# Kernel optimization log

Hardware: AMD Instinct MI355X
Metric: run time of the kernel (lower is better)

The kernel has to match this reference:

```python
import jax, jax.numpy as jnp
import numpy as np

B, T, H = 512, 32, 300


def setup_inputs() -> dict:
    key = jax.random.key(0)
    ks = jax.random.split(key, 24)
    u = lambda k, shape: jax.random.uniform(k, shape, jnp.float32, -0.1, 0.1)
    return {
        'local_inputs': jax.random.normal(ks[0], (B, T, 28, 10), jnp.float32),
        'labels': jax.random.normal(ks[1], (B, T, 1, 1), jnp.float32),
        'extras': jax.random.normal(ks[2], (B, T, 4, 1), jnp.float32),
        'DisM': jax.random.normal(ks[3], (10,), jnp.float32),
        'AngleM': jax.random.uniform(ks[4], (10,), jnp.float32, 0.0, 360.0),
        'Wih': u(ks[5], (10, 4 * H, 11)),
        'b_ih': u(ks[6], (10, 4 * H)),
        'b_hh': u(ks[7], (10, 4 * H)),
        'Wt': u(ks[8], (4 * H, 4)),
        'bt_ih': u(ks[9], (4 * H,)),
        'bt_hh': u(ks[10], (4 * H,)),
        'wp': u(ks[11], (H, 2 * H)),
        'bp': u(ks[12], (H, 1)),
        'F1': u(ks[13], (2 * H, 200)),
        'b1': u(ks[14], (200,)),
        'F2': u(ks[15], (202, 1)),
        'b2': u(ks[16], (1,)),
        'ff': u(ks[17], (100, 17)),
        'bff': u(ks[18], (100, 1)),
        'fuse1': u(ks[19], (H, 100)),
        'biasf': u(ks[20], (100,)),
        'Wout': u(ks[21], (100, 1)),
        'biasout': u(ks[22], (1,)),
        'a': u(ks[23], (1,)),
    }


def reference(local_inputs, labels, extras, DisM, AngleM,
              Wih, b_ih, b_hh, Wt, bt_ih, bt_hh,
              wp, bp, F1, b1, F2, b2, ff, bff,
              fuse1, biasf, Wout, biasout, a):
    x = jnp.transpose(local_inputs, (1, 0, 2, 3))   # [T,B,28,10]
    exs = jnp.transpose(extras, (1, 0, 2, 3))       # [T,B,4,1]
    labels_r = jnp.transpose(labels, (1, 0, 2, 3)).reshape(T, B, 1)
    b_cells = b_ih + b_hh                            # weight_hh * 0 vanishes; biases remain
    bt = bt_ih + bt_hh
    wA = jax.nn.softmax(DisM)                        # [10] static distance weights
    aa = a[0]

    def cells(s):  # s: [B,11,10] -> con [B,H,10]; zero-state LSTMCell per neighbor
        g = jnp.einsum('kgi,bik->bkg', Wih, s) + b_cells  # [B,10,4H]
        i, f, gg, o = jnp.split(g, 4, axis=-1)
        h = jax.nn.sigmoid(o) * jnp.tanh(jax.nn.sigmoid(i) * jnp.tanh(gg))
        return jnp.transpose(h, (0, 2, 1))

    def target_cell(t):  # [B,4] -> [B,H]
        g = t @ Wt.T + bt
        i, f, gg, o = jnp.split(g, 4, axis=-1)
        return jax.nn.sigmoid(o) * jnp.tanh(jax.nn.sigmoid(i) * jnp.tanh(gg))

    def attend_predict(fl, con1, htarget):
        # fl: [B,28,10], con1: [B,H,10]
        hcat = jnp.concatenate([jnp.transpose(con1, (0, 2, 1)),
                                jnp.broadcast_to(htarget[:, None, :], (B, 10, H))], axis=2)  # [B,10,2H]
        fc1 = jax.nn.relu(jnp.einsum('bkh,ho->bko', hcat, F1) + b1)          # [B,10,200]
        ang = jnp.abs(fl[:, 10, :] - AngleM[None, :]) / 360.0                # [B,10]
        fc2 = jnp.concatenate([fc1, fl[:, 8, :, None], ang[..., None]], axis=2)  # [B,10,202]
        wdyn = jax.nn.relu(jnp.einsum('bko,od->bkd', fc2, F2)[..., 0] + b2[0])   # [B,10]
        # faithful to the original: softmax over neighbors of [10,B], then FLAT reshape to [B,1,10]
        wa3 = jax.nn.softmax(wdyn.T, axis=0).reshape(B, 1, 10)
        cat = jnp.sum(con1 * wa3, axis=2)                                    # [B,H]
        flin2 = jnp.einsum('of,bfk->bok', ff, fl[:, 11:, :]) + bff           # [B,100,10]
        fusiondis = jnp.sum(flin2 * wA[None, None, :], axis=2)               # [B,100]
        fuse = cat @ fuse1 + biasf                                           # [B,100]
        return (aa * fuse + (1.0 - aa) * fusiondis) @ Wout + biasout         # [B,1]

    # t = 0: con1 = con (no lastcon yet)
    con0 = cells(x[0, :, :11, :])
    p0 = attend_predict(x[0], con0, target_cell(exs[0, :, :4, 0]))

    def step(lastcon, inp):
        fl, e = inp
        con = cells(fl[:, :11, :])
        ht = target_cell(e[:, :4, 0])
        con1 = jax.nn.relu(jnp.einsum('oh,bhk->bok', wp,
                                      jnp.concatenate([con, lastcon], axis=1)) + bp)  # [B,H,10]
        return con, attend_predict(fl, con1, ht)

    _, preds = jax.lax.scan(step, con0, (x[1:], exs[1:]))
    preds = jnp.concatenate([p0[None], preds], axis=0)  # [T,B,1]
    return preds, labels_r
```

## Files before the change

kernel.cpp:

```cpp
#include <hip/hip_runtime.h>
#include <hip/hip_bf16.h>


#define TB 3
#define NBT 171
#define NR 32
#define NTHR 512
#define NW 8
#define KP 616
#define TBF 16

#define OFF_SM    0
#define OFF_WBF2  163840
#define OFF_F1S   256256
#define OFF_WCELL 319488
#define OFF_BTP   392448
#define OFF_WTP   393348
#define OFF_F1F   396948
#define OFF_WA    414868
#define OFF_SWA   414878
#define BASE_U32  414880
#define CON1_BYTE ((size_t)BASE_U32 * 4)
#define CONG_BYTE (CON1_BYTE + (size_t)98304000)
#define WS_NEED_BYTES (CONG_BYTE + (size_t)98304000)

typedef __attribute__((ext_vector_type(8))) short s16x8;
typedef __attribute__((ext_vector_type(4))) float f32x4;
typedef unsigned short u16;

__device__ __forceinline__ float rcpf(float x){ return __builtin_amdgcn_rcpf(x); }
__device__ __forceinline__ float sigf(float x){ return rcpf(1.0f+__expf(-x)); }
__device__ __forceinline__ float tanhf_(float x){ return 1.0f - 2.0f*rcpf(__expf(2.0f*x)+1.0f); }
__device__ __forceinline__ float bfu(u16 u){ return __uint_as_float(((unsigned)u)<<16); }
__device__ __forceinline__ u16 f2us(float f){ return (u16)(__float_as_uint(f)>>16); }
__device__ __forceinline__ u16 f2usr(float f){
  __hip_bfloat16 h = __float2bfloat16(f);
  return *(u16*)&h;
}

__global__ __launch_bounds__(256,4) void kern_cells(
    const float* __restrict__ li, const float* wsf, u16* __restrict__ cong)
{
  __shared__ __align__(16) float xs[64][12];
  const int tid=threadIdx.x, k=blockIdx.x;
  const int tbase = blockIdx.y*64;
  const int t = tbase>>9, bg0 = tbase&511;
  for (int p=tid; p<64*11; p+=256){
    int r=p/11, i=p%11;
    xs[r][i] = li[(((size_t)(bg0+r)*32+t)*28+i)*10+k];
  }
  if (tid<64) xs[tid][11] = 1.0f;
  __syncthreads();
  const int w = tid>>6, lane = tid&63, lo=lane&15, qd=lane>>4;
  short av[8];
  #pragma unroll
  for (int j=0;j<8;j++){
    int kk = qd*8+j;
    float v = (kk<12)? xs[w*16+lo][kk] : 0.f;
    av[j] = (short)f2usr(v);
  }
  s16x8 Ax = (s16x8){av[0],av[1],av[2],av[3],av[4],av[5],av[6],av[7]};
  const unsigned* wc = (const unsigned*)wsf + OFF_WCELL;
  const s16x8 Z = (s16x8){0,0,0,0,0,0,0,0};
  for (int ht=0; ht<19; ht++){
    s16x8 Bi=Z, Bg=Z, Bo=Z;
    if (qd<2){
      const unsigned* bb = wc + (((k*19+ht)*3)*32 + qd*16+lo)*4;
      Bi = *(const s16x8*)(bb);
      Bg = *(const s16x8*)(bb + 32*4);
      Bo = *(const s16x8*)(bb + 64*4);
    }
    f32x4 gi={0.f,0.f,0.f,0.f}, gg={0.f,0.f,0.f,0.f}, go={0.f,0.f,0.f,0.f};
    gi = __builtin_amdgcn_mfma_f32_16x16x32_bf16(Ax, Bi, gi, 0,0,0);
    gg = __builtin_amdgcn_mfma_f32_16x16x32_bf16(Ax, Bg, gg, 0,0,0);
    go = __builtin_amdgcn_mfma_f32_16x16x32_bf16(Ax, Bo, go, 0,0,0);
    int h = ht*16+lo;
    if (h<300){
      #pragma unroll
      for (int r=0;r<4;r++){
        float hv = sigf(go[r]) * tanhf_( sigf(gi[r]) * tanhf_(gg[r]) );
        int tb = tbase + w*16 + qd*4 + r;
        cong[((size_t)tb*10+k)*300 + h] = f2usr(hv);
      }
    }
  }
}

__global__ __launch_bounds__(NTHR,8) void kern_main_split(
    const float* __restrict__ li, const float* __restrict__ exs,
    const float* __restrict__ AngleM, const float* __restrict__ bp,
    const float* __restrict__ F2, const float* __restrict__ b2,
    const float* wsf, unsigned* __restrict__ con1u, float* smg,
    const u16* __restrict__ cong)
{
  __shared__ __align__(16) u16 cct[NR][KP];
  __shared__ float xse[TB][2][10];
  __shared__ float exss[TB][4];
  __shared__ float wdP[NW][NR];
  __shared__ float wdL[NR];
  const int tid = threadIdx.x;
  const int t = blockIdx.y, bt = blockIdx.x, b0 = bt*TB;
  const int w = tid>>6, lane = tid&63, lo = lane&15, qd = lane>>4;

  for (int p=tid;p<TB*20;p+=NTHR){
    int b=p/20, r=p%20, rr=r/10, k=r%10;
    int bg = b0+b; if (bg>511) bg=511;
    xse[b][rr][k] = li[((bg*32+t)*28 + (rr?10:8))*10 + k];
  }
  for (int p=tid;p<TB*4;p+=NTHR){
    int b=p/4, e=p%4;
    int bg = b0+b; if (bg>511) bg=511;
    exss[b][e] = exs[(bg*32+t)*4+e];
  }
  for (int p=tid; p<30*4; p+=NTHR){
    int n=p/4, c=p%4;
    ((unsigned*)&cct[n][600])[c] = 0u;
  }
  __syncthreads();

  const int nh = (t==0)?1:2;
  for (int p=tid; p<nh*TB*750; p+=NTHR){
    int half=p/(TB*750), r=p%(TB*750), n=r/75, op=r%75;
    int tp = half? t-1 : t;
    int bg = b0 + n/10; if (bg>511) bg=511;
    uint2 v = *(const uint2*)((const unsigned*)cong +
                ((size_t)(tp*512+bg)*10 + n%10)*150 + 2*op);
    *(uint2*)((unsigned*)&cct[n][300*half] + 2*op) = v;
  }
  __syncthreads();

  f32x4 acc[3][2];
  #pragma unroll
  for (int i=0;i<3;i++)
    #pragma unroll
    for (int nt=0;nt<2;nt++) acc[i][nt] = (f32x4){0.f,0.f,0.f,0.f};
  if (t>0){
    const u16* wbfA = (const u16*)((const unsigned*)wsf + OFF_WBF2);
    for (int ks=0; ks<19; ks++){
      const int kb = ks*32 + qd*8;
      s16x8 Bv[2];
      #pragma unroll
      for (int nt=0;nt<2;nt++)
        Bv[nt] = *(const s16x8*)&cct[nt*16+lo][kb];
      #pragma unroll
      for (int i=0;i<3;i++){
        int mt = i*8+w;
        if (mt<19){
          s16x8 Av = *(const s16x8*)(wbfA + ((size_t)(mt*19+ks)*64 + lane)*8);
          #pragma unroll
          for (int nt=0;nt<2;nt++)
            acc[i][nt] = __builtin_amdgcn_mfma_f32_16x16x32_bf16(Av, Bv[nt], acc[i][nt], 0,0,0);
        }
      }
    }
  }
  __syncthreads();

  if (t>0){
    #pragma unroll
    for (int i=0;i<3;i++){
      int mt = i*8+w;
      if (mt<19 && (mt<18 || qd<3)){
        int ob = mt*16 + qd*4;
        float p0=bp[ob], p1=bp[ob+1], p2=bp[ob+2], p3=bp[ob+3];
        #pragma unroll
        for (int nt=0;nt<2;nt++){
          int n = nt*16+lo;
          float v0=acc[i][nt][0]+p0, v1=acc[i][nt][1]+p1,
                v2=acc[i][nt][2]+p2, v3=acc[i][nt][3]+p3;
          unsigned w0 = ((unsigned)f2us(v1>0.f?v1:0.f)<<16) | f2us(v0>0.f?v0:0.f);
          unsigned w1 = ((unsigned)f2us(v3>0.f?v3:0.f)<<16) | f2us(v2>0.f?v2:0.f);
          *(unsigned*)&cct[n][ob]   = w0;
          *(unsigned*)&cct[n][ob+2] = w1;
        }
      }
    }
  }
  for (int p=tid; p<TB*75; p+=NTHR){
    int b=p/75, q=p%75, o=4*q;
    f32x4 ai={0.f,0.f,0.f,0.f}, ag={0.f,0.f,0.f,0.f}, ao={0.f,0.f,0.f,0.f};
    #pragma unroll
    for (int e=0;e<4;e++){
      float xv = exss[b][e];
      f32x4 wi = *(const f32x4*)&wsf[OFF_WTP+(e*3+0)*300+o];
      f32x4 wg = *(const f32x4*)&wsf[OFF_WTP+(e*3+1)*300+o];
      f32x4 wo = *(const f32x4*)&wsf[OFF_WTP+(e*3+2)*300+o];
      #pragma unroll
      for (int c=0;c<4;c++){
        ai[c] += wi[c]*xv; ag[c] += wg[c]*xv; ao[c] += wo[c]*xv;
      }
    }
    f32x4 bi = *(const f32x4*)&wsf[OFF_BTP+o];
    f32x4 bg = *(const f32x4*)&wsf[OFF_BTP+300+o];
    f32x4 bo = *(const f32x4*)&wsf[OFF_BTP+600+o];
    u16 u[4];
    #pragma unroll
    for (int c=0;c<4;c++){
      float vi = ai[c]+bi[c], vg = ag[c]+bg[c], vo = ao[c]+bo[c];
      u[c] = f2usr( sigf(vo)*tanhf_(sigf(vi)*tanhf_(vg)) );
    }
    uint2 pk;
    pk.x = ((unsigned)u[1]<<16) | u[0];
    pk.y = ((unsigned)u[3]<<16) | u[2];
    #pragma unroll
    for (int k=0;k<10;k++)
      *(uint2*)&cct[b*10+k][300+o] = pk;
  }
  for (int p=tid; p<30*4; p+=NTHR){
    int n=p/4, c=p%4;
    ((unsigned*)&cct[n][600])[c] = (c==0)? 0x00003f80u : 0u;
  }
  __syncthreads();

  for (int p=tid; p<TB*750; p+=NTHR){
    int n=p/75, op=p%75;
    int bg = b0 + n/10;
    if (bg < 512){
      uint2 v = *(const uint2*)((unsigned*)&cct[n][0] + 2*op);
      *(uint2*)(con1u + ((size_t)(t*512+bg)*10 + n%10)*150 + 2*op) = v;
    }
  }

  f32x4 acc2[2][2];
  #pragma unroll
  for (int mt=0;mt<2;mt++)
    #pragma unroll
    for (int j=0;j<2;j++) acc2[mt][j] = (f32x4){0.f,0.f,0.f,0.f};
  {
    const u16* f1s = (const u16*)((const unsigned*)wsf + OFF_F1S);
    for (int ks=0; ks<19; ks++){
      const int kb = ks*32 + qd*8;
      s16x8 Am[2];
      #pragma unroll
      for (int mt=0;mt<2;mt++)
        Am[mt] = *(const s16x8*)&cct[mt*16+lo][kb];
      #pragma unroll
      for (int j=0;j<2;j++){
        int nt = w + j*8;
        if (nt<13){
          s16x8 Bf = *(const s16x8*)(f1s + ((size_t)(nt*19+ks)*64 + lane)*8);
          #pragma unroll
          for (int mt=0;mt<2;mt++)
            acc2[mt][j] = __builtin_amdgcn_mfma_f32_16x16x32_bf16(Am[mt], Bf, acc2[mt][j], 0,0,0);
        }
      }
    }
  }
  {
    float f2c[2];
    #pragma unroll
    for (int j=0;j<2;j++){
      int nt = w + j*8;
      int jj = nt*16+lo;
      f2c[j] = (nt<13 && jj<200)? F2[jj] : 0.f;
    }
    #pragma unroll
    for (int mt=0;mt<2;mt++)
      #pragma unroll
      for (int r=0;r<4;r++){
        float s = 0.f;
        #pragma unroll
        for (int j=0;j<2;j++){
          float v = acc2[mt][j][r];
          s += (v>0.f? v:0.f) * f2c[j];
        }
        s += __shfl_xor(s,1,64); s += __shfl_xor(s,2,64);
        s += __shfl_xor(s,4,64); s += __shfl_xor(s,8,64);
        if (lo==0) wdP[w][mt*16+qd*4+r] = s;
      }
  }
  __syncthreads();
  if (tid<TB*10){
    int n=tid, b=n/10, k=n%10;
    float v = 0.f;
    #pragma unroll
    for (int ww=0;ww<NW;ww++) v += wdP[ww][n];
    float ang = fabsf(xse[b][1][k]-AngleM[k]) * (1.0f/360.0f);
    v += xse[b][0][k]*F2[200] + ang*F2[201] + b2[0];
    wdL[n] = v>0.f? v : 0.f;
  }
  __syncthreads();
  if (tid<TB && b0+tid < 512){
    int b=tid;
    float m = wdL[b*10];
    #pragma unroll
    for (int k=1;k<10;k++) m = fmaxf(m, wdL[b*10+k]);
    float e[10]; float s=0.f;
    #pragma unroll
    for (int k=0;k<10;k++){ e[k]=__expf(wdL[b*10+k]-m); s+=e[k]; }
    float inv = rcpf(s);
    #pragma unroll
    for (int k=0;k<10;k++) smg[t*5120 + k*512 + b0+b] = e[k]*inv;
  }
}

__global__ __launch_bounds__(NTHR,8) void kern_final(
    const float* __restrict__ li, const float* __restrict__ labels,
    const float* __restrict__ ff, const float* __restrict__ bff,
    const float* __restrict__ biasf, const float* __restrict__ Wout,
    const float* __restrict__ biasout, const float* __restrict__ a,
    const float* wsf, const unsigned* __restrict__ con1u,
    float* __restrict__ outp)
{
  __shared__ __align__(16) float cats[TBF][324];
  __shared__ __align__(16) float xs17[TBF][17][10];
  __shared__ float wa3s[TBF][10];
  __shared__ float dss[TBF][17];
  __shared__ float wAs[10];
  __shared__ float part[7][TBF];
  const int tid=threadIdx.x, t=blockIdx.y, bt=blockIdx.x, b0=bt*TBF;
  const int w = tid>>6, lane = tid&63, lo = lane&15, qd = lane>>4;
  if (tid>=NTHR-TBF){
    int b = tid-(NTHR-TBF);
    outp[16384 + t*512 + b0+b] = labels[(b0+b)*32+t];
  }
  for (int p=tid;p<TBF*85;p+=NTHR){
    int b=p/85, r=p%85, f=r/5, pr=r%5;
    *(float2*)&xs17[b][f][2*pr] =
        *(const float2*)&li[(((b0+b)*32+t)*28 + 11+f)*10 + 2*pr];
  }
  if (tid<10) wAs[tid] = wsf[OFF_WA+tid];
  for (int p=tid;p<TBF*10;p+=NTHR){
    int b=p/10, k=p%10;
    int g = (b0+b)*10+k;
    wa3s[b][k] = wsf[OFF_SM + t*5120 + (g>>9)*512 + (g&511)];
  }
  __syncthreads();
  for (int p=tid;p<TBF*17;p+=NTHR){
    int b=p/17, f=p%17; float s=0.f;
    #pragma unroll
    for (int k=0;k<10;k++) s += xs17[b][f][k]*wAs[k];
    dss[b][f]=s;
  }
  for (int p=tid;p<TBF*75;p+=NTHR){
    int b=p/75, q=p%75, o=4*q;
    const unsigned* base = con1u + ((size_t)(t*512 + b0+b)*10)*150 + 2*q;
    f32x4 s = {0.f,0.f,0.f,0.f};
    #pragma unroll
    for (int k=0;k<10;k++){
      uint2 cv = *(const uint2*)(base + (size_t)k*150);
      float wk = wa3s[b][k];
      s[0] += bfu((u16)(cv.x & 0xffffu))*wk;
      s[1] += bfu((u16)(cv.x >> 16))*wk;
      s[2] += bfu((u16)(cv.y & 0xffffu))*wk;
      s[3] += bfu((u16)(cv.y >> 16))*wk;
    }
    *(f32x4*)&cats[b][o] = s;
  }
  for (int p=tid;p<TBF*6;p+=NTHR){
    int b=p/6, c=p%6;
    *(f32x4*)&cats[b][300+4*c] = (f32x4){0.f,0.f,0.f,0.f};
  }
  __syncthreads();
  if (w < 7){
    f32x4 D = (f32x4){0.f,0.f,0.f,0.f};
    const u16* f1f = (const u16*)((const unsigned*)wsf + OFF_F1F);
    for (int ks=0; ks<10; ks++){
      const int kb = ks*32 + qd*8;
      f32x4 c0 = *(const f32x4*)&cats[lo][kb];
      f32x4 c1 = *(const f32x4*)&cats[lo][kb+4];
      short av[8];
      #pragma unroll
      for (int j=0;j<4;j++){
        av[j]   = (short)f2usr(c0[j]);
        av[4+j] = (short)f2usr(c1[j]);
      }
      s16x8 Ax = (s16x8){av[0],av[1],av[2],av[3],av[4],av[5],av[6],av[7]};
      s16x8 Bf = *(const s16x8*)(f1f + ((size_t)(w*10+ks)*64 + lane)*8);
      D = __builtin_amdgcn_mfma_f32_16x16x32_bf16(Ax, Bf, D, 0,0,0);
    }
    {
      int o = w*16+lo;
      bool ov = o<100;
      float aa = a[0], swa = wsf[OFF_SWA];
      float bfo = ov? biasf[o] : 0.f;
      float bffo = ov? bff[o]*swa : 0.f;
      float wo = ov? Wout[o] : 0.f;
      #pragma unroll
      for (int r=0;r<4;r++){
        int b = qd*4+r;
        float fu = D[r] + bfo;
        float fd = bffo;
        if (ov){
          #pragma unroll
          for (int f=0;f<17;f++) fd += ff[o*17+f]*dss[b][f];
        }
        float v = (aa*fu + (1.f-aa)*fd) * wo;
        v += __shfl_xor(v,1,64); v += __shfl_xor(v,2,64);
        v += __shfl_xor(v,4,64); v += __shfl_xor(v,8,64);
        if (lo==0) part[w][b] = v;
      }
    }
  }
  __syncthreads();
  if (tid<TBF){
    int b=tid;
    float v = biasout[0];
    #pragma unroll
    for (int ww=0;ww<7;ww++) v += part[ww][b];
    outp[t*512 + b0+b] = v;
  }
}

__global__ void kprep(const float* __restrict__ Wih, const float* __restrict__ b_ih,
                      const float* __restrict__ b_hh, const float* __restrict__ Wt,
                      const float* __restrict__ bt_ih, const float* __restrict__ bt_hh,
                      const float* __restrict__ wp, const float* __restrict__ F1,
                      const float* __restrict__ b1, const float* __restrict__ fuse1,
                      const float* __restrict__ DisM, float* __restrict__ wsf)
{
  int n = blockIdx.x*256 + threadIdx.x;
  if (n < 92416){
    int jp=n&3, lane=(n>>2)&63, rest=n>>8;
    int ks=rest%19, mt=rest/19;
    int m = mt*16 + (lane&15);
    int k = ks*32 + (lane>>4)*8 + 2*jp;
    float v0 = (m<300 && k  <600)? wp[m*600+k  ] : 0.f;
    float v1 = (m<300 && k+1<600)? wp[m*600+k+1] : 0.f;
    ((unsigned*)wsf)[OFF_WBF2+n] = ((unsigned)f2usr(v1)<<16) | f2usr(v0);
    return;
  }
  n -= 92416;
  if (n < 63232){
    int jp=n&3, lane=(n>>2)&63, rest=n>>8;
    int ks=rest%19, nt=rest/19;
    int col = nt*16 + (lane&15);
    int k = ks*32 + (lane>>4)*8 + 2*jp;
    float v0=0.f, v1=0.f;
    if (col<200){
      v0 = (k  <600)? F1[k*200+col]     : (k  ==600? b1[col] : 0.f);
      v1 = (k+1<600)? F1[(k+1)*200+col] : (k+1==600? b1[col] : 0.f);
    }
    ((unsigned*)wsf)[OFF_F1S+n] = ((unsigned)f2usr(v1)<<16) | f2usr(v0);
    return;
  }
  n -= 63232;
  if (n < 72960){
    int jp=n&3, l32=(n>>2)&31, rest=n>>7;
    int g=rest%3, rest2=rest/3, ht=rest2%19, k=rest2/19;
    int lo=l32&15, q16=l32>>4;
    int h = ht*16 + lo;
    int kk0 = q16*8 + 2*jp;
    float v0=0.f, v1=0.f;
    if (h < 300){
      int G = h + (g==0?0:(g==1?600:900));
      v0 = (kk0  <11)? Wih[(k*1200+G)*11+kk0]
         : (kk0 ==11? b_ih[k*1200+G]+b_hh[k*1200+G] : 0.f);
      int kk1 = kk0+1;
      v1 = (kk1  <11)? Wih[(k*1200+G)*11+kk1]
         : (kk1 ==11? b_ih[k*1200+G]+b_hh[k*1200+G] : 0.f);
    }
    ((unsigned*)wsf)[OFF_WCELL+n] = ((unsigned)f2usr(v1)<<16) | f2usr(v0);
    return;
  }
  n -= 72960;
  if (n < 900){
    int h=n%300, g=n/300;
    int G = h + (g==0?0:(g==1?600:900));
    wsf[OFF_BTP+n] = bt_ih[G]+bt_hh[G]; return;
  }
  n -= 900;
  if (n < 3600){
    int h=n%300; int q=n/300; int g=q%3, e=q/3;
    int G = h + (g==0?0:(g==1?600:900));
    wsf[OFF_WTP+n] = Wt[G*4+e]; return;
  }
  n -= 3600;
  if (n < 17920){
    int jp=n&3, lane=(n>>2)&63, rest=n>>8;
    int ks=rest%10, nt=rest/10;
    int col = nt*16 + (lane&15);
    int kk0 = ks*32 + (lane>>4)*8 + 2*jp;
    float v0 = (col<100 && kk0  <300)? fuse1[kk0*100+col]     : 0.f;
    float v1 = (col<100 && kk0+1<300)? fuse1[(kk0+1)*100+col] : 0.f;
    ((unsigned*)wsf)[OFF_F1F+n] = ((unsigned)f2usr(v1)<<16) | f2usr(v0);
    return;
  }
  n -= 17920;
  if (n == 0){
    float m = DisM[0];
    for (int k=1;k<10;k++) m = fmaxf(m, DisM[k]);
    float e[10]; float s=0.f;
    for (int k=0;k<10;k++){ e[k]=__expf(DisM[k]-m); s+=e[k]; }
    float inv=1.0f/s; float sw=0.f;
    for (int k=0;k<10;k++){ float v=e[k]*inv; wsf[OFF_WA+k]=v; sw+=v; }
    wsf[OFF_SWA]=sw;
  }
}

extern "C" void kernel_launch(void* const* d_in, const int* in_sizes, int n_in,
                              void* d_out, int out_size, void* d_ws, size_t ws_size,
                              hipStream_t stream)
{
  const float* li     = (const float*)d_in[0];
  const float* labels = (const float*)d_in[1];
  const float* exs    = (const float*)d_in[2];
  const float* DisM   = (const float*)d_in[3];
  const float* AngleM = (const float*)d_in[4];
  const float* Wih    = (const float*)d_in[5];
  const float* b_ih   = (const float*)d_in[6];
  const float* b_hh   = (const float*)d_in[7];
  const float* Wt     = (const float*)d_in[8];
  const float* bt_ih  = (const float*)d_in[9];
  const float* bt_hh  = (const float*)d_in[10];
  const float* wp     = (const float*)d_in[11];
  const float* bp     = (const float*)d_in[12];
  const float* F1     = (const float*)d_in[13];
  const float* b1     = (const float*)d_in[14];
  const float* F2     = (const float*)d_in[15];
  const float* b2     = (const float*)d_in[16];
  const float* ff     = (const float*)d_in[17];
  const float* bff    = (const float*)d_in[18];
  const float* fuse1  = (const float*)d_in[19];
  const float* biasf  = (const float*)d_in[20];
  const float* Wout   = (const float*)d_in[21];
  const float* biasout= (const float*)d_in[22];
  const float* a      = (const float*)d_in[23];
  float* wsf = (float*)d_ws;
  float* outp = (float*)d_out;
  unsigned* con1u = (unsigned*)((char*)d_ws + CON1_BYTE);
  u16* cong = (u16*)((char*)d_ws + CONG_BYTE);

  if (ws_size < WS_NEED_BYTES) return;

  kprep<<<dim3(981), dim3(256), 0, stream>>>(Wih,b_ih,b_hh,Wt,bt_ih,bt_hh,wp,F1,b1,fuse1,DisM,wsf);
  kern_cells<<<dim3(10,256), dim3(256), 0, stream>>>(li, wsf, cong);
  kern_main_split<<<dim3(NBT,32), NTHR, 0, stream>>>(li, exs, AngleM, bp, F2, b2,
                                                     wsf, con1u, wsf + OFF_SM, cong);
  kern_final<<<dim3(32,32), NTHR, 0, stream>>>(li, labels, ff, bff, biasf,
                                               Wout, biasout, a, wsf, con1u, outp);
}
```

Measured before the change: 394.0 us.

## Vectorize cell output stores via lane shuffles and restructure main-kernel row copies

In the cell kernel, MFMA outputs are transposed across lanes with xor shuffles so each lane writes four consecutive bf16 values as one 8-byte store, replacing scattered 2-byte stores. In the main kernel, the global-to-LDS copy of neighbour rows and the LDS-to-global copy of con1 are reorganised so each wavefront moves one row, removing per-element div/mod. The target-cell LSTM computation is hoisted before the wp GEMM and kept in registers, and one barrier is dropped. This adds shuffle instructions and register pressure in exchange for wider, more coalesced memory traffic.

Result: no change. 394.6 us (+0.1%).

```diff
diff --git a/kernel.cpp b/kernel.cpp
--- a/kernel.cpp
+++ b/kernel.cpp
@@ -52,6 +52,7 @@
   if (tid<64) xs[tid][11] = 1.0f;
   __syncthreads();
   const int w = tid>>6, lane = tid&63, lo=lane&15, qd=lane>>4;
+  const int c4 = lane&3;
   short av[8];
   #pragma unroll
   for (int j=0;j<8;j++){
@@ -62,6 +63,7 @@
   s16x8 Ax = (s16x8){av[0],av[1],av[2],av[3],av[4],av[5],av[6],av[7]};
   const unsigned* wc = (const unsigned*)wsf + OFF_WCELL;
   const s16x8 Z = (s16x8){0,0,0,0,0,0,0,0};
+  const size_t rowbase = ((size_t)(tbase + w*16 + qd*4 + c4)*10 + k)*300;
   for (int ht=0; ht<19; ht++){
     s16x8 Bi=Z, Bg=Z, Bo=Z;
     if (qd<2){
@@ -74,14 +76,32 @@
     gi = __builtin_amdgcn_mfma_f32_16x16x32_bf16(Ax, Bi, gi, 0,0,0);
     gg = __builtin_amdgcn_mfma_f32_16x16x32_bf16(Ax, Bg, gg, 0,0,0);
     go = __builtin_amdgcn_mfma_f32_16x16x32_bf16(Ax, Bo, go, 0,0,0);
-    int h = ht*16+lo;
-    if (h<300){
-      #pragma unroll
-      for (int r=0;r<4;r++){
-        float hv = sigf(go[r]) * tanhf_( sigf(gi[r]) * tanhf_(gg[r]) );
-        int tb = tbase + w*16 + qd*4 + r;
-        cong[((size_t)tb*10+k)*300 + h] = f2usr(hv);
-      }
+    float v0 = sigf(go[0]) * tanhf_( sigf(gi[0]) * tanhf_(gg[0]) );
+    float v1 = sigf(go[1]) * tanhf_( sigf(gi[1]) * tanhf_(gg[1]) );
+    float v2 = sigf(go[2]) * tanhf_( sigf(gi[2]) * tanhf_(gg[2]) );
+    float v3 = sigf(go[3]) * tanhf_( sigf(gi[3]) * tanhf_(gg[3]) );
+    {
+      bool hiC = (lane & 2) != 0;
+      float s0 = hiC ? v0 : v2;
+      float s1 = hiC ? v1 : v3;
+      float r0 = __shfl_xor(s0, 2, 64);
+      float r1 = __shfl_xor(s1, 2, 64);
+      if (hiC){ v0 = r0; v1 = r1; } else { v2 = r0; v3 = r1; }
+    }
+    {
+      bool odd = (lane & 1) != 0;
+      float s0 = odd ? v0 : v1;
+      float s1 = odd ? v2 : v3;
+      float r0 = __shfl_xor(s0, 1, 64);
+      float r1 = __shfl_xor(s1, 1, 64);
+      if (odd){ v0 = r0; v2 = r1; } else { v1 = r0; v3 = r1; }
+    }
+    int g = (lane>>2)&3;
+    if (!(ht==18 && g==3)){
+      uint2 pk;
+      pk.x = ((unsigned)f2usr(v1)<<16) | f2usr(v0);
+      pk.y = ((unsigned)f2usr(v3)<<16) | f2usr(v2);
+      *(uint2*)&cong[rowbase + ht*16 + 4*g] = pk;
     }
   }
 }
@@ -116,18 +136,55 @@
     int n=p/4, c=p%4;
     ((unsigned*)&cct[n][600])[c] = 0u;
   }
-  __syncthreads();
 
   const int nh = (t==0)?1:2;
-  for (int p=tid; p<nh*TB*750; p+=NTHR){
-    int half=p/(TB*750), r=p%(TB*750), n=r/75, op=r%75;
+  for (int half=0; half<nh; half++){
     int tp = half? t-1 : t;
-    int bg = b0 + n/10; if (bg>511) bg=511;
-    uint2 v = *(const uint2*)((const unsigned*)cong +
-                ((size_t)(tp*512+bg)*10 + n%10)*150 + 2*op);
-    *(uint2*)((unsigned*)&cct[n][300*half] + 2*op) = v;
-  }
-  __syncthreads();
+    for (int u=w; u<30; u+=NW){
+      int b = (u>=20)?2:((u>=10)?1:0);
+      int kk = u - b*10;
+      int bg = b0+b; if (bg>511) bg=511;
+      const unsigned* src = (const unsigned*)cong +
+            ((size_t)(tp*512+bg)*10 + kk)*150;
+      unsigned* dst = (unsigned*)&cct[u][300*half];
+      uint2 v = *(const uint2*)(src + 2*lane);
+      *(uint2*)(dst + 2*lane) = v;
+      if (lane<11){
+        uint2 v2 = *(const uint2*)(src + 2*(lane+64));
+        *(uint2*)(dst + 2*(lane+64)) = v2;
+      }
+    }
+  }
+  __syncthreads();
+
+  uint2 pk3; int b3=0, o3=0; const bool h3 = (tid < TB*75);
+  if (h3){
+    b3 = (tid>=150)?2:((tid>=75)?1:0);
+    o3 = 4*(tid - b3*75);
+    f32x4 ai={0.f,0.f,0.f,0.f}, ag={0.f,0.f,0.f,0.f}, ao={0.f,0.f,0.f,0.f};
+    #pragma unroll
+    for (int e=0;e<4;e++){
+      float xv = exss[b3][e];
+      f32x4 wi = *(const f32x4*)&wsf[OFF_WTP+(e*3+0)*300+o3];
+      f32x4 wg = *(const f32x4*)&wsf[OFF_WTP+(e*3+1)*300+o3];
+      f32x4 wo = *(const f32x4*)&wsf[OFF_WTP+(e*3+2)*300+o3];
+      #pragma unroll
+      for (int c=0;c<4;c++){
+        ai[c] += wi[c]*xv; ag[c] += wg[c]*xv; ao[c] += wo[c]*xv;
+      }
+    }
+    f32x4 bi = *(const f32x4*)&wsf[OFF_BTP+o3];
+    f32x4 bg = *(const f32x4*)&wsf[OFF_BTP+300+o3];
+    f32x4 bo = *(const f32x4*)&wsf[OFF_BTP+600+o3];
+    u16 u[4];
+    #pragma unroll
+    for (int c=0;c<4;c++){
+      float vi = ai[c]+bi[c], vg = ag[c]+bg[c], vo = ao[c]+bo[c];
+      u[c] = f2usr( sigf(vo)*tanhf_(sigf(vi)*tanhf_(vg)) );
+    }
+    pk3.x = ((unsigned)u[1]<<16) | u[0];
+    pk3.y = ((unsigned)u[3]<<16) | u[2];
+  }
 
   f32x4 acc[3][2];
   #pragma unroll
@@ -176,35 +233,10 @@
       }
     }
   }
-  for (int p=tid; p<TB*75; p+=NTHR){
-    int b=p/75, q=p%75, o=4*q;
-    f32x4 ai={0.f,0.f,0.f,0.f}, ag={0.f,0.f,0.f,0.f}, ao={0.f,0.f,0.f,0.f};
-    #pragma unroll
-    for (int e=0;e<4;e++){
-      float xv = exss[b][e];
-      f32x4 wi = *(const f32x4*)&wsf[OFF_WTP+(e*3+0)*300+o];
-      f32x4 wg = *(const f32x4*)&wsf[OFF_WTP+(e*3+1)*300+o];
-      f32x4 wo = *(const f32x4*)&wsf[OFF_WTP+(e*3+2)*300+o];
-      #pragma unroll
-      for (int c=0;c<4;c++){
-        ai[c] += wi[c]*xv; ag[c] += wg[c]*xv; ao[c] += wo[c]*xv;
-      }
-    }
-    f32x4 bi = *(const f32x4*)&wsf[OFF_BTP+o];
-    f32x4 bg = *(const f32x4*)&wsf[OFF_BTP+300+o];
-    f32x4 bo = *(const f32x4*)&wsf[OFF_BTP+600+o];
-    u16 u[4];
-    #pragma unroll
-    for (int c=0;c<4;c++){
-      float vi = ai[c]+bi[c], vg = ag[c]+bg[c], vo = ao[c]+bo[c];
-      u[c] = f2usr( sigf(vo)*tanhf_(sigf(vi)*tanhf_(vg)) );
-    }
-    uint2 pk;
-    pk.x = ((unsigned)u[1]<<16) | u[0];
-    pk.y = ((unsigned)u[3]<<16) | u[2];
+  if (h3){
     #pragma unroll
     for (int k=0;k<10;k++)
-      *(uint2*)&cct[b*10+k][300+o] = pk;
+      *(uint2*)&cct[b3*10+k][300+o3] = pk3;
   }
   for (int p=tid; p<30*4; p+=NTHR){
     int n=p/4, c=p%4;
@@ -212,12 +244,19 @@
   }
   __syncthreads();
 
-  for (int p=tid; p<TB*750; p+=NTHR){
-    int n=p/75, op=p%75;
-    int bg = b0 + n/10;
-    if (bg < 512){
-      uint2 v = *(const uint2*)((unsigned*)&cct[n][0] + 2*op);
-      *(uint2*)(con1u + ((size_t)(t*512+bg)*10 + n%10)*150 + 2*op) = v;
+  for (int u=w; u<30; u+=NW){
+    int b = (u>=20)?2:((u>=10)?1:0);
+    int bg = b0+b;
+    if (bg<512){
+      int kk = u - b*10;
+      unsigned* dst = con1u + ((size_t)(t*512+bg)*10 + kk)*150;
+      const unsigned* src = (const unsigned*)&cct[u][0];
+      uint2 v = *(const uint2*)(src + 2*lane);
+      *(uint2*)(dst + 2*lane) = v;
+      if (lane<11){
+        uint2 v2 = *(const uint2*)(src + 2*(lane+64));
+        *(uint2*)(dst + 2*(lane+64)) = v2;
+      }
     }
   }
 
```

## Transpose MFMA outputs via lane shuffles for packed stores, remap block order

Applied to the files above, without the earlier changes.

In the cell kernel, each lane's 4-row MFMA accumulator is transposed across lanes with two xor-shuffle rounds. Each lane then holds 4 consecutive hidden units of one row and writes them as a single 8-byte packed bf16 store, replacing four scattered 2-byte stores. This is meant to cut the number of uncoalesced global writes to the intermediate buffer. Separately, the main kernel remaps its linear block index so that blocks scheduled together (likely on different XCDs) work on nearby batch/time tiles, aiming at better L2 locality at the cost of a less obvious index mapping.

Result: faster. 382.4 us (-3.0%).

```diff
diff --git a/kernel.cpp b/kernel.cpp
--- a/kernel.cpp
+++ b/kernel.cpp
@@ -52,6 +52,7 @@
   if (tid<64) xs[tid][11] = 1.0f;
   __syncthreads();
   const int w = tid>>6, lane = tid&63, lo=lane&15, qd=lane>>4;
+  const int c4 = lane&3;
   short av[8];
   #pragma unroll
   for (int j=0;j<8;j++){
@@ -62,6 +63,7 @@
   s16x8 Ax = (s16x8){av[0],av[1],av[2],av[3],av[4],av[5],av[6],av[7]};
   const unsigned* wc = (const unsigned*)wsf + OFF_WCELL;
   const s16x8 Z = (s16x8){0,0,0,0,0,0,0,0};
+  const size_t rowbase = ((size_t)(tbase + w*16 + qd*4 + c4)*10 + k)*300;
   for (int ht=0; ht<19; ht++){
     s16x8 Bi=Z, Bg=Z, Bo=Z;
     if (qd<2){
@@ -74,14 +76,32 @@
     gi = __builtin_amdgcn_mfma_f32_16x16x32_bf16(Ax, Bi, gi, 0,0,0);
     gg = __builtin_amdgcn_mfma_f32_16x16x32_bf16(Ax, Bg, gg, 0,0,0);
     go = __builtin_amdgcn_mfma_f32_16x16x32_bf16(Ax, Bo, go, 0,0,0);
-    int h = ht*16+lo;
-    if (h<300){
-      #pragma unroll
-      for (int r=0;r<4;r++){
-        float hv = sigf(go[r]) * tanhf_( sigf(gi[r]) * tanhf_(gg[r]) );
-        int tb = tbase + w*16 + qd*4 + r;
-        cong[((size_t)tb*10+k)*300 + h] = f2usr(hv);
-      }
+    float v0 = sigf(go[0]) * tanhf_( sigf(gi[0]) * tanhf_(gg[0]) );
+    float v1 = sigf(go[1]) * tanhf_( sigf(gi[1]) * tanhf_(gg[1]) );
+    float v2 = sigf(go[2]) * tanhf_( sigf(gi[2]) * tanhf_(gg[2]) );
+    float v3 = sigf(go[3]) * tanhf_( sigf(gi[3]) * tanhf_(gg[3]) );
+    {
+      bool hiC = (lane & 2) != 0;
+      float s0 = hiC ? v0 : v2;
+      float s1 = hiC ? v1 : v3;
+      float r0 = __shfl_xor(s0, 2, 64);
+      float r1 = __shfl_xor(s1, 2, 64);
+      if (hiC){ v0 = r0; v1 = r1; } else { v2 = r0; v3 = r1; }
+    }
+    {
+      bool odd = (lane & 1) != 0;
+      float s0 = odd ? v0 : v1;
+      float s1 = odd ? v2 : v3;
+      float r0 = __shfl_xor(s0, 1, 64);
+      float r1 = __shfl_xor(s1, 1, 64);
+      if (odd){ v0 = r0; v2 = r1; } else { v1 = r0; v3 = r1; }
+    }
+    int g = (lane>>2)&3;
+    if (!(ht==18 && g==3)){
+      uint2 pk;
+      pk.x = ((unsigned)f2usr(v1)<<16) | f2usr(v0);
+      pk.y = ((unsigned)f2usr(v3)<<16) | f2usr(v2);
+      *(uint2*)&cong[rowbase + ht*16 + 4*g] = pk;
     }
   }
 }
@@ -99,7 +119,9 @@
   __shared__ float wdP[NW][NR];
   __shared__ float wdL[NR];
   const int tid = threadIdx.x;
-  const int t = blockIdx.y, bt = blockIdx.x, b0 = bt*TB;
+  const int L = blockIdx.x + NBT*blockIdx.y;
+  const int virt = (L&7)*684 + (L>>3);
+  const int bt = virt>>5, t = virt&31, b0 = bt*TB;
   const int w = tid>>6, lane = tid&63, lo = lane&15, qd = lane>>4;
 
   for (int p=tid;p<TB*20;p+=NTHR){
```
